# Optimization experiments

Measured on AMD Instinct MI355X. Metric: run time of the kernel, lower is better.

## Reference

```python
import jax, jax.numpy as jnp
import numpy as np
from jax import lax

# dims: B=2, C=dim=64, H=W=128 -> N=16384 tokens; d_inner=128, d_state=16, dt_rank=4, d_conv=4

def setup_inputs() -> dict:
    key = jax.random.key(0)
    ks = jax.random.split(key, 8)
    def n(k, shp, scale=0.02):
        return jax.random.normal(k, shp, jnp.float32) * scale
    d_inner, d_state, dt_rank = 128, 16, 4
    return {
        "x": jax.random.normal(ks[0], (2, 64, 128, 128), jnp.float32),
        "ln_w": jnp.ones((64,), jnp.float32),
        "ln_b": jnp.zeros((64,), jnp.float32),
        "in_proj_w": n(ks[1], (2 * d_inner, 64)),
        "conv_w": n(ks[2], (d_inner, 1, 4), 0.1),
        "conv_b": jnp.zeros((d_inner,), jnp.float32),
        "x_proj_w": n(ks[3], (dt_rank + 2 * d_state, d_inner)),
        "dt_proj_w": n(ks[4], (d_inner, dt_rank), 0.5),
        "dt_proj_b": n(ks[5], (d_inner,), 0.1),
        "A_log": jnp.log(jnp.broadcast_to(jnp.arange(1, d_state + 1, dtype=jnp.float32), (d_inner, d_state))),
        "D_param": jnp.ones((d_inner,), jnp.float32),
        "out_proj_w": n(ks[6], (64, d_inner)),
        "out_proj_b": jnp.zeros((64,), jnp.float32),
    }


def reference(x, ln_w, ln_b, in_proj_w, conv_w, conv_b, x_proj_w,
              dt_proj_w, dt_proj_b, A_log, D_param, out_proj_w, out_proj_b):
    B, C, H, W = x.shape
    d_inner = in_proj_w.shape[0] // 2
    d_state = A_log.shape[1]
    dt_rank = dt_proj_w.shape[1]
    eps = 1e-5

    # feature2token + channel LayerNorm (Restormer WithBias LN over C)
    t = x.reshape(B, C, H * W).transpose(0, 2, 1)  # [B, N, C]
    mu = jnp.mean(t, axis=-1, keepdims=True)
    var = jnp.var(t, axis=-1, keepdims=True)
    t = (t - mu) * lax.rsqrt(var + eps) * ln_w + ln_b

    # in_proj -> x, z
    xz = jnp.einsum('bnc,dc->bnd', t, in_proj_w)  # [B, N, 2*d_inner]
    x_in, z = jnp.split(xz, 2, axis=-1)

    # depthwise causal conv1d (k=4, pad left 3), then SiLU
    u = lax.conv_general_dilated(
        x_in.transpose(0, 2, 1), conv_w,
        window_strides=(1,), padding=[(3, 0)],
        feature_group_count=d_inner,
        dimension_numbers=('NCH', 'OIH', 'NCH'))
    u = jax.nn.silu(u + conv_b[None, :, None]).transpose(0, 2, 1)  # [B, N, d_inner]

    # x_proj -> dt, B, C of the SSM
    x_dbl = jnp.einsum('bnd,ed->bne', u, x_proj_w)
    dt_r = x_dbl[..., :dt_rank]
    Bmat = x_dbl[..., dt_rank:dt_rank + d_state]   # [B, N, d_state]
    Cmat = x_dbl[..., dt_rank + d_state:]          # [B, N, d_state]
    dt = jax.nn.softplus(jnp.einsum('bnr,dr->bnd', dt_r, dt_proj_w) + dt_proj_b)

    # selective scan: h_t = exp(dt*A) h_{t-1} + dt*B*u
    A = -jnp.exp(A_log)  # [d_inner, d_state]
    deltaA = jnp.exp(jnp.einsum('bnd,ds->bnds', dt, A))
    deltaBu = jnp.einsum('bnd,bns,bnd->bnds', dt, Bmat, u)

    def combine(c1, c2):
        a1, b1 = c1
        a2, b2 = c2
        return a2 * a1, a2 * b1 + b2

    _, h = lax.associative_scan(combine, (deltaA, deltaBu), axis=1)  # h: [B, N, d_inner, d_state]

    y = jnp.einsum('bnds,bns->bnd', h, Cmat) + u * D_param
    y = y * jax.nn.silu(z)
    out = jnp.einsum('bnd,cd->bnc', y, out_proj_w) + out_proj_b  # [B, N, C]

    # token2feature
    return out.transpose(0, 2, 1).reshape(B, C, H, W)
```

## Files before the change

kernel.cpp:

```cpp
#include <hip/hip_runtime.h>
#include <math.h>

#define NTOK 16384
#define DIN  128
#define NCH  512
#define CHL  32
#define NG   32
#define GCH  16

__device__ __forceinline__ float silu_f(float x)    { return x / (1.f + __expf(-x)); }
__device__ __forceinline__ float softplus_f(float x){ return (x > 20.f) ? x : log1pf(__expf(x)); }

__global__ __launch_bounds__(256) void k1_ln_inproj(
    const float* __restrict__ x, const float* __restrict__ lnw,
    const float* __restrict__ lnb, const float* __restrict__ Win,
    float* __restrict__ xin, float* __restrict__ zbuf)
{
  __shared__ __align__(16) float bufA[128*68];
  __shared__ __align__(16) float bufB[64*68];
  __shared__ float ps[256], pq[256], mu[64], rs[64];

  int t = threadIdx.x;
  int b  = blockIdx.x >> 8;
  int n0 = (blockIdx.x & 255) << 6;
  const float* xb = x + ((size_t)b*64)*NTOK;

  int tok = t & 63, quad = t >> 6;
  float s0 = 0.f, s1 = 0.f;
  for (int i = 0; i < 16; ++i) {
    int c = i*4 + quad;
    float v = xb[(size_t)c*NTOK + n0 + tok];
    bufA[c*68 + tok] = v;
    s0 += v; s1 += v*v;
  }
  ps[t] = s0; pq[t] = s1;
  __syncthreads();
  if (t < 64) {
    float m = ps[t] + ps[64+t] + ps[128+t] + ps[192+t];
    float q = pq[t] + pq[64+t] + pq[128+t] + pq[192+t];
    m *= 0.015625f;
    q = q*0.015625f - m*m;
    mu[t] = m; rs[t] = rsqrtf(q + 1e-5f);
  }
  __syncthreads();

  {
    int c = t & 63, tq = t >> 6;
    float wv = lnw[c], bv = lnb[c];
    const float4* A4 = (const float4*)bufA;
    #pragma unroll
    for (int i = 0; i < 4; ++i) {
      int tok4 = tq*4 + i;
      float4 f = A4[c*17 + tok4];
      float vals[4] = {f.x, f.y, f.z, f.w};
      #pragma unroll
      for (int k = 0; k < 4; ++k) {
        int tk = tok4*4 + k;
        bufB[tk*68 + c] = (vals[k] - mu[tk]) * rs[tk] * wv + bv;
      }
    }
  }

  int tokg = t & 15, dg = t >> 4;
  for (int half = 0; half < 2; ++half) {
    __syncthreads();
    for (int i = 0; i < 32; ++i) {
      int idx = i*256 + t;
      int c = idx & 63, dd = idx >> 6;
      bufA[dd*68 + c] = Win[((half<<7) + dd)*64 + c];
    }
    __syncthreads();
    float acc[4][8];
    #pragma unroll
    for (int i = 0; i < 4; ++i)
      #pragma unroll
      for (int j = 0; j < 8; ++j) acc[i][j] = 0.f;
    const float4* TB = (const float4*)bufB;
    const float4* WA = (const float4*)bufA;
    #pragma unroll 4
    for (int c4 = 0; c4 < 16; ++c4) {
      float4 tv[4], wv[8];
      #pragma unroll
      for (int i = 0; i < 4; ++i) tv[i] = TB[(tokg + 16*i)*17 + c4];
      #pragma unroll
      for (int j = 0; j < 8; ++j) wv[j] = WA[(dg + 16*j)*17 + c4];
      #pragma unroll
      for (int i = 0; i < 4; ++i)
        #pragma unroll
        for (int j = 0; j < 8; ++j)
          acc[i][j] += tv[i].x*wv[j].x + tv[i].y*wv[j].y
                     + tv[i].z*wv[j].z + tv[i].w*wv[j].w;
    }
    #pragma unroll
    for (int i = 0; i < 4; ++i) {
      long n = (long)b*NTOK + n0 + tokg + 16*i;
      #pragma unroll
      for (int j = 0; j < 8; ++j) {
        int d = dg + 16*j;
        if (half == 0) xin[n*128 + d] = acc[i][j];
        else           zbuf[n*128 + d] = silu_f(acc[i][j]);
      }
    }
  }
}

__global__ __launch_bounds__(256) void k2_conv(
    const float* __restrict__ xin, const float* __restrict__ cw,
    const float* __restrict__ cb, float* __restrict__ u)
{
  int t = threadIdx.x;
  int d = t & 127;
  long g0 = (long)blockIdx.x*16 + (t >> 7)*8;
  int n = (int)(g0 & (NTOK-1));
  float w0 = cw[d*4], w1 = cw[d*4+1], w2 = cw[d*4+2], w3 = cw[d*4+3];
  float cbv = cb[d];
  float xa = (n >= 3) ? xin[(g0-3)*128 + d] : 0.f;
  float xb = (n >= 2) ? xin[(g0-2)*128 + d] : 0.f;
  float xc = (n >= 1) ? xin[(g0-1)*128 + d] : 0.f;
  #pragma unroll
  for (int j = 0; j < 8; ++j) {
    float xd = xin[(g0+j)*128 + d];
    u[(g0+j)*128 + d] = silu_f(w0*xa + w1*xb + w2*xc + w3*xd + cbv);
    xa = xb; xb = xc; xc = xd;
  }
}

__global__ __launch_bounds__(256) void k3_xproj_dt(
    const float* __restrict__ u, const float* __restrict__ Wx,
    const float* __restrict__ Wdt, const float* __restrict__ db,
    float* __restrict__ dt, float* __restrict__ Bm, float* __restrict__ Cm)
{
  __shared__ __align__(16) float wx[36*128];
  __shared__ float wdtT[4*128];
  __shared__ __align__(16) float xdbl[64*40];
  int t = threadIdx.x;
  for (int i = t; i < 1152; i += 256)
    *(float4*)&wx[i*4] = *(const float4*)&Wx[i*4];
  for (int i = t; i < 512; i += 256)
    wdtT[(i&3)*128 + (i>>2)] = Wdt[i];
  __syncthreads();

  long tok0 = (long)blockIdx.x * 64;
  int tok = t & 63, grp = t >> 6;
  const float* urow = u + (tok0 + tok)*128;

  float acc[9];
  #pragma unroll
  for (int e = 0; e < 9; ++e) acc[e] = 0.f;
  #pragma unroll 8
  for (int d4 = 0; d4 < 32; ++d4) {
    float4 uv = *(const float4*)&urow[d4*4];
    #pragma unroll
    for (int e = 0; e < 9; ++e) {
      float4 wv = *(const float4*)&wx[(grp*9+e)*128 + d4*4];
      acc[e] += uv.x*wv.x + uv.y*wv.y + uv.z*wv.z + uv.w*wv.w;
    }
  }
  #pragma unroll
  for (int e = 0; e < 9; ++e) xdbl[tok*40 + grp*9 + e] = acc[e];
  __syncthreads();

  {
    int tk = t >> 2, q = t & 3;
    float4 bv = *(const float4*)&xdbl[tk*40 + 4  + q*4];
    float4 cv = *(const float4*)&xdbl[tk*40 + 20 + q*4];
    *(float4*)&Bm[(tok0+tk)*16 + q*4] = bv;
    *(float4*)&Cm[(tok0+tk)*16 + q*4] = cv;
  }
  int d = t & 127, th = t >> 7;
  float w0 = wdtT[d], w1 = wdtT[128+d], w2 = wdtT[256+d], w3 = wdtT[384+d];
  float bias = db[d];
  for (int j = 0; j < 32; ++j) {
    int tk = th*32 + j;
    float a = bias + xdbl[tk*40]*w0 + xdbl[tk*40+1]*w1
                   + xdbl[tk*40+2]*w2 + xdbl[tk*40+3]*w3;
    dt[(tok0+tk)*128 + d] = softplus_f(a);
  }
}

__global__ __launch_bounds__(128) void k4a_local(
    const float* __restrict__ dt, const float* __restrict__ u,
    const float* __restrict__ Bm, const float* __restrict__ Alog,
    float* __restrict__ carP, float* __restrict__ carH)
{
  int d = threadIdx.x;
  int b = blockIdx.x / NCH, ch = blockIdx.x % NCH;
  long nb = (long)b*NTOK + (long)ch*CHL;
  float A[16], h[16], P[16];
  #pragma unroll
  for (int k = 0; k < 4; ++k) {
    float4 a = *(const float4*)&Alog[d*16 + k*4];
    A[k*4+0] = -__expf(a.x); A[k*4+1] = -__expf(a.y);
    A[k*4+2] = -__expf(a.z); A[k*4+3] = -__expf(a.w);
  }
  #pragma unroll
  for (int s = 0; s < 16; ++s) { h[s] = 0.f; P[s] = 1.f; }
  for (int i = 0; i < CHL; ++i) {
    long n = nb + i;
    float dtv = dt[n*128 + d];
    float uv  = u [n*128 + d];
    float du  = dtv * uv;
    float Bv[16];
    #pragma unroll
    for (int k = 0; k < 4; ++k) {
      float4 v = *(const float4*)&Bm[n*16 + k*4];
      Bv[k*4]=v.x; Bv[k*4+1]=v.y; Bv[k*4+2]=v.z; Bv[k*4+3]=v.w;
    }
    #pragma unroll
    for (int s = 0; s < 16; ++s) {
      float dA = __expf(dtv * A[s]);
      h[s] = dA*h[s] + du*Bv[s];
      P[s] *= dA;
    }
  }
  long cbs = ((long)(b*NCH + ch)*128 + d) * 16;
  #pragma unroll
  for (int k = 0; k < 4; ++k) {
    *(float4*)&carP[cbs + k*4] = make_float4(P[k*4],P[k*4+1],P[k*4+2],P[k*4+3]);
    *(float4*)&carH[cbs + k*4] = make_float4(h[k*4],h[k*4+1],h[k*4+2],h[k*4+3]);
  }
}

__global__ __launch_bounds__(256) void k4b1_group(
    float* __restrict__ cP, float* __restrict__ cH,
    float* __restrict__ Pg, float* __restrict__ Hg)
{
  int idx = blockIdx.x*256 + threadIdx.x;
  int rem = idx & 2047;
  int g   = (idx >> 11) & (NG-1);
  int b   = idx >> 16;
  float P = 1.f, H = 0.f;
  long base = ((long)b*NCH + g*GCH)*2048 + rem;
  #pragma unroll 4
  for (int j = 0; j < GCH; ++j) {
    long a = base + (long)j*2048;
    float p = cP[a], h = cH[a];
    cP[a] = P; cH[a] = H;
    H = p*H + h;
    P = p*P;
  }
  long ga = ((long)b*NG + g)*2048 + rem;
  Pg[ga] = P; Hg[ga] = H;
}

__global__ __launch_bounds__(256) void k4b2_carry(
    const float* __restrict__ Pg, float* __restrict__ Hg)
{
  int idx = blockIdx.x*256 + threadIdx.x;
  int b = idx >> 11, rem = idx & 2047;
  float H = 0.f;
  #pragma unroll 4
  for (int g = 0; g < NG; ++g) {
    long a = ((long)b*NG + g)*2048 + rem;
    float p = Pg[a], h = Hg[a];
    Hg[a] = H;
    H = p*H + h;
  }
}

__global__ __launch_bounds__(128) void k4c_apply(
    const float* __restrict__ dt, const float* __restrict__ u,
    const float* __restrict__ Bm, const float* __restrict__ Cm,
    const float* __restrict__ Alog, const float* __restrict__ Dp,
    const float* __restrict__ zs, const float* __restrict__ pPre,
    const float* __restrict__ hPre, const float* __restrict__ Hg,
    float* __restrict__ yz)
{
  int d = threadIdx.x;
  int b = blockIdx.x / NCH, ch = blockIdx.x % NCH;
  long nb = (long)b*NTOK + (long)ch*CHL;
  float A[16], h[16];
  #pragma unroll
  for (int k = 0; k < 4; ++k) {
    float4 a = *(const float4*)&Alog[d*16 + k*4];
    A[k*4+0] = -__expf(a.x); A[k*4+1] = -__expf(a.y);
    A[k*4+2] = -__expf(a.z); A[k*4+3] = -__expf(a.w);
  }
  long cbs = ((long)(b*NCH + ch)*128 + d) * 16;
  long gbs = ((long)b*NG + (ch >> 4))*2048 + d*16;
  #pragma unroll
  for (int k = 0; k < 4; ++k) {
    float4 hp = *(const float4*)&hPre[cbs + k*4];
    float4 pp = *(const float4*)&pPre[cbs + k*4];
    float4 gi = *(const float4*)&Hg[gbs + k*4];
    h[k*4+0] = hp.x + pp.x*gi.x; h[k*4+1] = hp.y + pp.y*gi.y;
    h[k*4+2] = hp.z + pp.z*gi.z; h[k*4+3] = hp.w + pp.w*gi.w;
  }
  float Dv = Dp[d];
  for (int i = 0; i < CHL; ++i) {
    long n = nb + i;
    float dtv = dt[n*128 + d];
    float uv  = u [n*128 + d];
    float du  = dtv * uv;
    float Bv[16], Cv[16];
    #pragma unroll
    for (int k = 0; k < 4; ++k) {
      float4 v = *(const float4*)&Bm[n*16 + k*4];
      Bv[k*4]=v.x; Bv[k*4+1]=v.y; Bv[k*4+2]=v.z; Bv[k*4+3]=v.w;
      float4 w = *(const float4*)&Cm[n*16 + k*4];
      Cv[k*4]=w.x; Cv[k*4+1]=w.y; Cv[k*4+2]=w.z; Cv[k*4+3]=w.w;
    }
    float y = 0.f;
    #pragma unroll
    for (int s = 0; s < 16; ++s) {
      float dA = __expf(dtv * A[s]);
      h[s] = dA*h[s] + du*Bv[s];
      y += h[s]*Cv[s];
    }
    y = (y + uv*Dv) * zs[n*128 + d];
    yz[n*128 + d] = y;
  }
}

__global__ __launch_bounds__(256) void k6_outproj(
    const float* __restrict__ yz, const float* __restrict__ Wout,
    const float* __restrict__ ob, float* __restrict__ out)
{
  __shared__ __align__(16) float wo[64*132];
  __shared__ __align__(16) float yl[32*132];
  int t = threadIdx.x;
  long tok0 = (long)blockIdx.x * 32;
  for (int i = 0; i < 8; ++i) {
    int g = i*256 + t; int c = g >> 5, q = g & 31;
    *(float4*)&wo[c*132 + q*4] = *(const float4*)&Wout[c*128 + q*4];
  }
  for (int i = 0; i < 4; ++i) {
    int g = i*256 + t; int tok = g >> 5, q = g & 31;
    *(float4*)&yl[tok*132 + q*4] = *(const float4*)&yz[(tok0 + tok)*128 + q*4];
  }
  __syncthreads();
  int tp = t & 15;
  int tg = t >> 4;
  float acc[4][2] = {{0.f}};
  for (int d4 = 0; d4 < 32; ++d4) {
    float4 y0 = *(const float4*)&yl[tg*132 + d4*4];
    float4 y1 = *(const float4*)&yl[(tg+16)*132 + d4*4];
    #pragma unroll
    for (int cc = 0; cc < 4; ++cc) {
      float4 wv = *(const float4*)&wo[(tp + 16*cc)*132 + d4*4];
      acc[cc][0] += wv.x*y0.x + wv.y*y0.y + wv.z*y0.z + wv.w*y0.w;
      acc[cc][1] += wv.x*y1.x + wv.y*y1.y + wv.z*y1.z + wv.w*y1.w;
    }
  }
  int b  = (int)(tok0 / NTOK);
  long n0 = tok0 % NTOK;
  #pragma unroll
  for (int cc = 0; cc < 4; ++cc) {
    int c = tp + 16*cc;
    float bias = ob[c];
    out[((long)b*64 + c)*NTOK + n0 + tg     ] = acc[cc][0] + bias;
    out[((long)b*64 + c)*NTOK + n0 + tg + 16] = acc[cc][1] + bias;
  }
}

extern "C" void kernel_launch(void* const* d_in, const int* in_sizes, int n_in,
                              void* d_out, int out_size, void* d_ws, size_t ws_size,
                              hipStream_t stream)
{
  (void)in_sizes; (void)n_in; (void)out_size; (void)ws_size;
  const float* x    = (const float*)d_in[0];
  const float* lnw  = (const float*)d_in[1];
  const float* lnb  = (const float*)d_in[2];
  const float* Win  = (const float*)d_in[3];
  const float* cw   = (const float*)d_in[4];
  const float* cb   = (const float*)d_in[5];
  const float* Wx   = (const float*)d_in[6];
  const float* Wdt  = (const float*)d_in[7];
  const float* db   = (const float*)d_in[8];
  const float* Alog = (const float*)d_in[9];
  const float* Dp   = (const float*)d_in[10];
  const float* Wout = (const float*)d_in[11];
  const float* ob   = (const float*)d_in[12];
  float* out = (float*)d_out;

  float* w   = (float*)d_ws;
  float* xin = w;
  float* z   = w + 4194304;
  float* u   = w + 8388608;
  float* dt  = w + 12582912;
  float* Bm  = w + 16777216;
  float* Cm  = w + 17301504;
  float* cP  = w + 17825792;
  float* cH  = w + 19922944;
  float* Pg  = w + 22020096;
  float* Hg  = w + 22151168;

  k1_ln_inproj<<<512, 256, 0, stream>>>(x, lnw, lnb, Win, xin, z);
  k2_conv     <<<2048,256, 0, stream>>>(xin, cw, cb, u);
  k3_xproj_dt <<<512, 256, 0, stream>>>(u, Wx, Wdt, db, dt, Bm, Cm);
  k4a_local   <<<1024,128, 0, stream>>>(dt, u, Bm, Alog, cP, cH);
  k4b1_group  <<<512, 256, 0, stream>>>(cP, cH, Pg, Hg);
  k4b2_carry  <<<16,  256, 0, stream>>>(Pg, Hg);
  k4c_apply   <<<1024,128, 0, stream>>>(dt, u, Bm, Cm, Alog, Dp, z, cP, cH, Hg, xin);
  k6_outproj  <<<1024,256, 0, stream>>>(xin, Wout, ob, out);
}
```

Baseline: 158.0 us.

## Fuse causal conv into LN/in_proj kernel and out_proj into scan apply

The conv1d stage moves into the LayerNorm/in_proj kernel. Each block now recomputes LN and the x projection for three halo tokens and runs the depthwise conv from shared memory, so the xin intermediate is never written to or read from global memory. The out projection is fused into the scan-apply kernel, which stages y in shared memory and writes the output directly, removing the yz round trip and two launches. The cost is redundant halo computation and more shared memory per block, including 8K floats of Wout loaded per apply block, which may lower occupancy.

```diff
diff --git a/kernel.cpp b/kernel.cpp
--- a/kernel.cpp
+++ b/kernel.cpp
@@ -11,77 +11,94 @@
 __device__ __forceinline__ float silu_f(float x)    { return x / (1.f + __expf(-x)); }
 __device__ __forceinline__ float softplus_f(float x){ return (x > 20.f) ? x : log1pf(__expf(x)); }
 
-__global__ __launch_bounds__(256) void k1_ln_inproj(
+__global__ __launch_bounds__(256) void k12(
     const float* __restrict__ x, const float* __restrict__ lnw,
     const float* __restrict__ lnb, const float* __restrict__ Win,
-    float* __restrict__ xin, float* __restrict__ zbuf)
-{
-  __shared__ __align__(16) float bufA[128*68];
-  __shared__ __align__(16) float bufB[64*68];
-  __shared__ float ps[256], pq[256], mu[64], rs[64];
+    const float* __restrict__ cw, const float* __restrict__ cb,
+    float* __restrict__ zbuf, float* __restrict__ u)
+{
+  __shared__ __align__(16) float bufA[128*69];
+  __shared__ __align__(16) float bufB[67*68];
+  __shared__ float ps[256], pq[256];
+  __shared__ float mu[67], rs[67];
 
   int t = threadIdx.x;
   int b  = blockIdx.x >> 8;
   int n0 = (blockIdx.x & 255) << 6;
-  const float* xb = x + ((size_t)b*64)*NTOK;
+  const float* xb = x + (size_t)b*64*NTOK;
 
   int tok = t & 63, quad = t >> 6;
   float s0 = 0.f, s1 = 0.f;
   for (int i = 0; i < 16; ++i) {
     int c = i*4 + quad;
     float v = xb[(size_t)c*NTOK + n0 + tok];
-    bufA[c*68 + tok] = v;
+    bufA[c*68 + tok + 3] = v;
     s0 += v; s1 += v*v;
   }
   ps[t] = s0; pq[t] = s1;
-  __syncthreads();
+  float vh = 0.f;
+  if (t < 192) {
+    int c = t & 63, k = t >> 6;
+    int n = n0 - 3 + k;
+    vh = (n >= 0) ? xb[(size_t)c*NTOK + n] : 0.f;
+    bufA[c*68 + k] = vh;
+  }
+  __syncthreads();
+  if (t < 192) {
+    float a0 = vh, a1 = vh*vh;
+    #pragma unroll
+    for (int m = 1; m < 64; m <<= 1) { a0 += __shfl_xor(a0, m); a1 += __shfl_xor(a1, m); }
+    if ((t & 63) == 0) {
+      int k = t >> 6;
+      float m = a0 * 0.015625f;
+      float q = a1 * 0.015625f - m*m;
+      mu[k] = m; rs[k] = rsqrtf(q + 1e-5f);
+    }
+  }
   if (t < 64) {
     float m = ps[t] + ps[64+t] + ps[128+t] + ps[192+t];
     float q = pq[t] + pq[64+t] + pq[128+t] + pq[192+t];
     m *= 0.015625f;
     q = q*0.015625f - m*m;
-    mu[t] = m; rs[t] = rsqrtf(q + 1e-5f);
-  }
-  __syncthreads();
-
+    mu[t+3] = m; rs[t+3] = rsqrtf(q + 1e-5f);
+  }
+  __syncthreads();
   {
     int c = t & 63, tq = t >> 6;
     float wv = lnw[c], bv = lnb[c];
-    const float4* A4 = (const float4*)bufA;
-    #pragma unroll
-    for (int i = 0; i < 4; ++i) {
-      int tok4 = tq*4 + i;
-      float4 f = A4[c*17 + tok4];
-      float vals[4] = {f.x, f.y, f.z, f.w};
-      #pragma unroll
-      for (int k = 0; k < 4; ++k) {
-        int tk = tok4*4 + k;
-        bufB[tk*68 + c] = (vals[k] - mu[tk]) * rs[tk] * wv + bv;
+    #pragma unroll
+    for (int i = 0; i < 17; ++i) {
+      int tp = tq + 4*i;
+      if (tp < 67) {
+        float val = (tp < 3 && n0 == 0) ? 0.f
+                  : (bufA[c*68 + tp] - mu[tp]) * rs[tp] * wv + bv;
+        bufB[tp*68 + c] = val;
       }
     }
   }
 
   int tokg = t & 15, dg = t >> 4;
-  for (int half = 0; half < 2; ++half) {
-    __syncthreads();
-    for (int i = 0; i < 32; ++i) {
-      int idx = i*256 + t;
-      int c = idx & 63, dd = idx >> 6;
-      bufA[dd*68 + c] = Win[((half<<7) + dd)*64 + c];
-    }
-    __syncthreads();
+  const float4* TB = (const float4*)bufB;
+
+  __syncthreads();
+  for (int i = 0; i < 32; ++i) {
+    int idx = i*256 + t;
+    int c = idx & 63, dd = idx >> 6;
+    bufA[dd*68 + c] = Win[(128 + dd)*64 + c];
+  }
+  __syncthreads();
+  {
+    const float4* WA = (const float4*)bufA;
     float acc[4][8];
     #pragma unroll
     for (int i = 0; i < 4; ++i)
       #pragma unroll
       for (int j = 0; j < 8; ++j) acc[i][j] = 0.f;
-    const float4* TB = (const float4*)bufB;
-    const float4* WA = (const float4*)bufA;
     #pragma unroll 4
     for (int c4 = 0; c4 < 16; ++c4) {
       float4 tv[4], wv[8];
       #pragma unroll
-      for (int i = 0; i < 4; ++i) tv[i] = TB[(tokg + 16*i)*17 + c4];
+      for (int i = 0; i < 4; ++i) tv[i] = TB[(3 + tokg + 16*i)*17 + c4];
       #pragma unroll
       for (int j = 0; j < 8; ++j) wv[j] = WA[(dg + 16*j)*17 + c4];
       #pragma unroll
@@ -95,33 +112,73 @@
     for (int i = 0; i < 4; ++i) {
       long n = (long)b*NTOK + n0 + tokg + 16*i;
       #pragma unroll
-      for (int j = 0; j < 8; ++j) {
-        int d = dg + 16*j;
-        if (half == 0) xin[n*128 + d] = acc[i][j];
-        else           zbuf[n*128 + d] = silu_f(acc[i][j]);
+      for (int j = 0; j < 8; ++j)
+        zbuf[n*128 + dg + 16*j] = silu_f(acc[i][j]);
+    }
+  }
+
+  __syncthreads();
+  for (int i = 0; i < 32; ++i) {
+    int idx = i*256 + t;
+    int c = idx & 63, dd = idx >> 6;
+    bufA[dd*68 + c] = Win[dd*64 + c];
+  }
+  __syncthreads();
+  float acc[4][8], acch[8];
+  {
+    const float4* WA = (const float4*)bufA;
+    #pragma unroll
+    for (int i = 0; i < 4; ++i)
+      #pragma unroll
+      for (int j = 0; j < 8; ++j) acc[i][j] = 0.f;
+    #pragma unroll
+    for (int j = 0; j < 8; ++j) acch[j] = 0.f;
+    #pragma unroll 4
+    for (int c4 = 0; c4 < 16; ++c4) {
+      float4 tv[4], wv[8];
+      #pragma unroll
+      for (int i = 0; i < 4; ++i) tv[i] = TB[(3 + tokg + 16*i)*17 + c4];
+      #pragma unroll
+      for (int j = 0; j < 8; ++j) wv[j] = WA[(dg + 16*j)*17 + c4];
+      #pragma unroll
+      for (int i = 0; i < 4; ++i)
+        #pragma unroll
+        for (int j = 0; j < 8; ++j)
+          acc[i][j] += tv[i].x*wv[j].x + tv[i].y*wv[j].y
+                     + tv[i].z*wv[j].z + tv[i].w*wv[j].w;
+      if (tokg < 3) {
+        float4 th = TB[tokg*17 + c4];
+        #pragma unroll
+        for (int j = 0; j < 8; ++j)
+          acch[j] += th.x*wv[j].x + th.y*wv[j].y + th.z*wv[j].z + th.w*wv[j].w;
       }
     }
   }
-}
-
-__global__ __launch_bounds__(256) void k2_conv(
-    const float* __restrict__ xin, const float* __restrict__ cw,
-    const float* __restrict__ cb, float* __restrict__ u)
-{
-  int t = threadIdx.x;
-  int d = t & 127;
-  long g0 = (long)blockIdx.x*16 + (t >> 7)*8;
-  int n = (int)(g0 & (NTOK-1));
-  float w0 = cw[d*4], w1 = cw[d*4+1], w2 = cw[d*4+2], w3 = cw[d*4+3];
-  float cbv = cb[d];
-  float xa = (n >= 3) ? xin[(g0-3)*128 + d] : 0.f;
-  float xb = (n >= 2) ? xin[(g0-2)*128 + d] : 0.f;
-  float xc = (n >= 1) ? xin[(g0-1)*128 + d] : 0.f;
-  #pragma unroll
-  for (int j = 0; j < 8; ++j) {
-    float xd = xin[(g0+j)*128 + d];
-    u[(g0+j)*128 + d] = silu_f(w0*xa + w1*xb + w2*xc + w3*xd + cbv);
-    xa = xb; xb = xc; xc = xd;
+  __syncthreads();
+  #pragma unroll
+  for (int i = 0; i < 4; ++i)
+    #pragma unroll
+    for (int j = 0; j < 8; ++j)
+      bufA[(dg + 16*j)*69 + 3 + tokg + 16*i] = acc[i][j];
+  if (tokg < 3)
+    #pragma unroll
+    for (int j = 0; j < 8; ++j)
+      bufA[(dg + 16*j)*69 + tokg] = acch[j];
+  __syncthreads();
+
+  {
+    int d = t & 127, th = t >> 7;
+    float w0 = cw[d*4], w1 = cw[d*4+1], w2 = cw[d*4+2], w3 = cw[d*4+3];
+    float cbv = cb[d];
+    int base = d*69 + th*32;
+    float xa = bufA[base], xb2 = bufA[base+1], xc = bufA[base+2];
+    long g0 = (long)b*NTOK + n0 + th*32;
+    #pragma unroll
+    for (int j = 0; j < 32; ++j) {
+      float xd = bufA[base + j + 3];
+      u[(g0 + j)*128 + d] = silu_f(w0*xa + w1*xb2 + w2*xc + w3*xd + cbv);
+      xa = xb2; xb2 = xc; xc = xd;
+    }
   }
 }
 
@@ -258,15 +315,24 @@
   }
 }
 
-__global__ __launch_bounds__(128) void k4c_apply(
+__global__ __launch_bounds__(128) void k46(
     const float* __restrict__ dt, const float* __restrict__ u,
     const float* __restrict__ Bm, const float* __restrict__ Cm,
     const float* __restrict__ Alog, const float* __restrict__ Dp,
     const float* __restrict__ zs, const float* __restrict__ pPre,
     const float* __restrict__ hPre, const float* __restrict__ Hg,
-    float* __restrict__ yz)
-{
-  int d = threadIdx.x;
+    const float* __restrict__ Wout, const float* __restrict__ ob,
+    float* __restrict__ out)
+{
+  __shared__ __align__(16) float yl[32*132];
+  __shared__ __align__(16) float wo[64*128];
+  int t = threadIdx.x;
+  for (int i = 0; i < 16; ++i) {
+    int idx = i*128 + t;
+    *(float4*)&wo[idx*4] = *(const float4*)&Wout[idx*4];
+  }
+
+  int d = t;
   int b = blockIdx.x / NCH, ch = blockIdx.x % NCH;
   long nb = (long)b*NTOK + (long)ch*CHL;
   float A[16], h[16];
@@ -307,49 +373,30 @@
       h[s] = dA*h[s] + du*Bv[s];
       y += h[s]*Cv[s];
     }
-    y = (y + uv*Dv) * zs[n*128 + d];
-    yz[n*128 + d] = y;
-  }
-}
-
-__global__ __launch_bounds__(256) void k6_outproj(
-    const float* __restrict__ yz, const float* __restrict__ Wout,
-    const float* __restrict__ ob, float* __restrict__ out)
-{
-  __shared__ __align__(16) float wo[64*132];
-  __shared__ __align__(16) float yl[32*132];
-  int t = threadIdx.x;
-  long tok0 = (long)blockIdx.x * 32;
-  for (int i = 0; i < 8; ++i) {
-    int g = i*256 + t; int c = g >> 5, q = g & 31;
-    *(float4*)&wo[c*132 + q*4] = *(const float4*)&Wout[c*128 + q*4];
-  }
-  for (int i = 0; i < 4; ++i) {
-    int g = i*256 + t; int tok = g >> 5, q = g & 31;
-    *(float4*)&yl[tok*132 + q*4] = *(const float4*)&yz[(tok0 + tok)*128 + q*4];
-  }
-  __syncthreads();
-  int tp = t & 15;
-  int tg = t >> 4;
-  float acc[4][2] = {{0.f}};
-  for (int d4 = 0; d4 < 32; ++d4) {
-    float4 y0 = *(const float4*)&yl[tg*132 + d4*4];
-    float4 y1 = *(const float4*)&yl[(tg+16)*132 + d4*4];
-    #pragma unroll
-    for (int cc = 0; cc < 4; ++cc) {
-      float4 wv = *(const float4*)&wo[(tp + 16*cc)*132 + d4*4];
-      acc[cc][0] += wv.x*y0.x + wv.y*y0.y + wv.z*y0.z + wv.w*y0.w;
-      acc[cc][1] += wv.x*y1.x + wv.y*y1.y + wv.z*y1.z + wv.w*y1.w;
-    }
-  }
-  int b  = (int)(tok0 / NTOK);
-  long n0 = tok0 % NTOK;
-  #pragma unroll
-  for (int cc = 0; cc < 4; ++cc) {
-    int c = tp + 16*cc;
-    float bias = ob[c];
-    out[((long)b*64 + c)*NTOK + n0 + tg     ] = acc[cc][0] + bias;
-    out[((long)b*64 + c)*NTOK + n0 + tg + 16] = acc[cc][1] + bias;
+    yl[i*132 + d] = (y + uv*Dv) * zs[n*128 + d];
+  }
+  __syncthreads();
+
+  {
+    int tok = t & 31, cg = t >> 5;
+    float acc[16];
+    #pragma unroll
+    for (int cc = 0; cc < 16; ++cc) acc[cc] = 0.f;
+    #pragma unroll 4
+    for (int d4 = 0; d4 < 32; ++d4) {
+      float4 yv = *(const float4*)&yl[tok*132 + d4*4];
+      #pragma unroll
+      for (int cc = 0; cc < 16; ++cc) {
+        float4 wv = *(const float4*)&wo[(cg*16+cc)*128 + d4*4];
+        acc[cc] += yv.x*wv.x + yv.y*wv.y + yv.z*wv.z + yv.w*wv.w;
+      }
+    }
+    long col = (long)ch*CHL + tok;
+    #pragma unroll
+    for (int cc = 0; cc < 16; ++cc) {
+      int c = cg*16 + cc;
+      out[((long)b*64 + c)*NTOK + col] = acc[cc] + ob[c];
+    }
   }
 }
 
@@ -374,23 +421,21 @@
   float* out = (float*)d_out;
 
   float* w   = (float*)d_ws;
-  float* xin = w;
-  float* z   = w + 4194304;
-  float* u   = w + 8388608;
-  float* dt  = w + 12582912;
-  float* Bm  = w + 16777216;
-  float* Cm  = w + 17301504;
-  float* cP  = w + 17825792;
-  float* cH  = w + 19922944;
-  float* Pg  = w + 22020096;
-  float* Hg  = w + 22151168;
-
-  k1_ln_inproj<<<512, 256, 0, stream>>>(x, lnw, lnb, Win, xin, z);
-  k2_conv     <<<2048,256, 0, stream>>>(xin, cw, cb, u);
-  k3_xproj_dt <<<512, 256, 0, stream>>>(u, Wx, Wdt, db, dt, Bm, Cm);
-  k4a_local   <<<1024,128, 0, stream>>>(dt, u, Bm, Alog, cP, cH);
-  k4b1_group  <<<512, 256, 0, stream>>>(cP, cH, Pg, Hg);
-  k4b2_carry  <<<16,  256, 0, stream>>>(Pg, Hg);
-  k4c_apply   <<<1024,128, 0, stream>>>(dt, u, Bm, Cm, Alog, Dp, z, cP, cH, Hg, xin);
-  k6_outproj  <<<1024,256, 0, stream>>>(xin, Wout, ob, out);
-}
+  float* z   = w;
+  float* u   = w + 4194304;
+  float* dt  = w + 8388608;
+  float* Bm  = w + 12582912;
+  float* Cm  = w + 13107200;
+  float* cP  = w + 13631488;
+  float* cH  = w + 15728640;
+  float* Pg  = w + 17825792;
+  float* Hg  = w + 17956864;
+
+  k12        <<<512, 256, 0, stream>>>(x, lnw, lnb, Win, cw, cb, z, u);
+  k3_xproj_dt<<<512, 256, 0, stream>>>(u, Wx, Wdt, db, dt, Bm, Cm);
+  k4a_local  <<<1024,128, 0, stream>>>(dt, u, Bm, Alog, cP, cH);
+  k4b1_group <<<512, 256, 0, stream>>>(cP, cH, Pg, Hg);
+  k4b2_carry <<<16,  256, 0, stream>>>(Pg, Hg);
+  k46        <<<1024,128, 0, stream>>>(dt, u, Bm, Cm, Alog, Dp, z, cP, cH, Hg,
+                                       Wout, ob, out);
+}
```

Measured after the change: 182.7 us. 1.16x slower.

## Split scan state across thread pairs and quarter in_proj weight tiles

Applied to the files above, without the earlier changes.

The scan kernels now assign two threads per channel, each owning 8 of the 16 state elements, with the output reduced by a lane shuffle. This doubles the thread count and halves per-thread serial work and registers. k1 processes in_proj in four 64-row weight tiles instead of two 128-row ones, halving the shared-memory buffer and accumulator count to improve occupancy. The scan output goes to a separate yz buffer instead of overwriting xin, which adds workspace use, and each thread pair loads dt and u redundantly.

```diff
diff --git a/kernel.cpp b/kernel.cpp
--- a/kernel.cpp
+++ b/kernel.cpp
@@ -16,7 +16,7 @@
     const float* __restrict__ lnb, const float* __restrict__ Win,
     float* __restrict__ xin, float* __restrict__ zbuf)
 {
-  __shared__ __align__(16) float bufA[128*68];
+  __shared__ __align__(16) float bufA[64*68];
   __shared__ __align__(16) float bufB[64*68];
   __shared__ float ps[256], pq[256], mu[64], rs[64];
 
@@ -47,11 +47,10 @@
   {
     int c = t & 63, tq = t >> 6;
     float wv = lnw[c], bv = lnb[c];
-    const float4* A4 = (const float4*)bufA;
     #pragma unroll
     for (int i = 0; i < 4; ++i) {
       int tok4 = tq*4 + i;
-      float4 f = A4[c*17 + tok4];
+      float4 f = *(const float4*)&bufA[c*68 + tok4*4];
       float vals[4] = {f.x, f.y, f.z, f.w};
       #pragma unroll
       for (int k = 0; k < 4; ++k) {
@@ -62,32 +61,32 @@
   }
 
   int tokg = t & 15, dg = t >> 4;
-  for (int half = 0; half < 2; ++half) {
+  const float4* TB = (const float4*)bufB;
+  for (int q = 0; q < 4; ++q) {
     __syncthreads();
-    for (int i = 0; i < 32; ++i) {
+    for (int i = 0; i < 16; ++i) {
       int idx = i*256 + t;
       int c = idx & 63, dd = idx >> 6;
-      bufA[dd*68 + c] = Win[((half<<7) + dd)*64 + c];
+      bufA[dd*68 + c] = Win[(q*64 + dd)*64 + c];
     }
     __syncthreads();
-    float acc[4][8];
+    const float4* WA = (const float4*)bufA;
+    float acc[4][4];
     #pragma unroll
     for (int i = 0; i < 4; ++i)
       #pragma unroll
-      for (int j = 0; j < 8; ++j) acc[i][j] = 0.f;
-    const float4* TB = (const float4*)bufB;
-    const float4* WA = (const float4*)bufA;
+      for (int j = 0; j < 4; ++j) acc[i][j] = 0.f;
     #pragma unroll 4
     for (int c4 = 0; c4 < 16; ++c4) {
-      float4 tv[4], wv[8];
+      float4 tv[4], wv[4];
       #pragma unroll
       for (int i = 0; i < 4; ++i) tv[i] = TB[(tokg + 16*i)*17 + c4];
       #pragma unroll
-      for (int j = 0; j < 8; ++j) wv[j] = WA[(dg + 16*j)*17 + c4];
+      for (int j = 0; j < 4; ++j) wv[j] = WA[(dg + 16*j)*17 + c4];
       #pragma unroll
       for (int i = 0; i < 4; ++i)
         #pragma unroll
-        for (int j = 0; j < 8; ++j)
+        for (int j = 0; j < 4; ++j)
           acc[i][j] += tv[i].x*wv[j].x + tv[i].y*wv[j].y
                      + tv[i].z*wv[j].z + tv[i].w*wv[j].w;
     }
@@ -95,10 +94,10 @@
     for (int i = 0; i < 4; ++i) {
       long n = (long)b*NTOK + n0 + tokg + 16*i;
       #pragma unroll
-      for (int j = 0; j < 8; ++j) {
-        int d = dg + 16*j;
-        if (half == 0) xin[n*128 + d] = acc[i][j];
-        else           zbuf[n*128 + d] = silu_f(acc[i][j]);
+      for (int j = 0; j < 4; ++j) {
+        int dd = dg + 16*j;
+        if (q < 2) xin[n*128 + q*64 + dd] = acc[i][j];
+        else       zbuf[n*128 + (q-2)*64 + dd] = silu_f(acc[i][j]);
       }
     }
   }
@@ -178,44 +177,45 @@
   }
 }
 
-__global__ __launch_bounds__(128) void k4a_local(
+__global__ __launch_bounds__(256) void k4a_local(
     const float* __restrict__ dt, const float* __restrict__ u,
     const float* __restrict__ Bm, const float* __restrict__ Alog,
     float* __restrict__ carP, float* __restrict__ carH)
 {
-  int d = threadIdx.x;
+  int t = threadIdx.x;
+  int d = t >> 1, sh = t & 1;
   int b = blockIdx.x / NCH, ch = blockIdx.x % NCH;
   long nb = (long)b*NTOK + (long)ch*CHL;
-  float A[16], h[16], P[16];
-  #pragma unroll
-  for (int k = 0; k < 4; ++k) {
-    float4 a = *(const float4*)&Alog[d*16 + k*4];
+  float A[8], h[8], P[8];
+  #pragma unroll
+  for (int k = 0; k < 2; ++k) {
+    float4 a = *(const float4*)&Alog[d*16 + sh*8 + k*4];
     A[k*4+0] = -__expf(a.x); A[k*4+1] = -__expf(a.y);
     A[k*4+2] = -__expf(a.z); A[k*4+3] = -__expf(a.w);
   }
   #pragma unroll
-  for (int s = 0; s < 16; ++s) { h[s] = 0.f; P[s] = 1.f; }
+  for (int s = 0; s < 8; ++s) { h[s] = 0.f; P[s] = 1.f; }
   for (int i = 0; i < CHL; ++i) {
     long n = nb + i;
     float dtv = dt[n*128 + d];
     float uv  = u [n*128 + d];
     float du  = dtv * uv;
-    float Bv[16];
-    #pragma unroll
-    for (int k = 0; k < 4; ++k) {
-      float4 v = *(const float4*)&Bm[n*16 + k*4];
+    float Bv[8];
+    #pragma unroll
+    for (int k = 0; k < 2; ++k) {
+      float4 v = *(const float4*)&Bm[n*16 + sh*8 + k*4];
       Bv[k*4]=v.x; Bv[k*4+1]=v.y; Bv[k*4+2]=v.z; Bv[k*4+3]=v.w;
     }
     #pragma unroll
-    for (int s = 0; s < 16; ++s) {
+    for (int s = 0; s < 8; ++s) {
       float dA = __expf(dtv * A[s]);
       h[s] = dA*h[s] + du*Bv[s];
       P[s] *= dA;
     }
   }
-  long cbs = ((long)(b*NCH + ch)*128 + d) * 16;
-  #pragma unroll
-  for (int k = 0; k < 4; ++k) {
+  long cbs = ((long)(b*NCH + ch)*128 + d)*16 + sh*8;
+  #pragma unroll
+  for (int k = 0; k < 2; ++k) {
     *(float4*)&carP[cbs + k*4] = make_float4(P[k*4],P[k*4+1],P[k*4+2],P[k*4+3]);
     *(float4*)&carH[cbs + k*4] = make_float4(h[k*4],h[k*4+1],h[k*4+2],h[k*4+3]);
   }
@@ -258,7 +258,7 @@
   }
 }
 
-__global__ __launch_bounds__(128) void k4c_apply(
+__global__ __launch_bounds__(256) void k4c_apply(
     const float* __restrict__ dt, const float* __restrict__ u,
     const float* __restrict__ Bm, const float* __restrict__ Cm,
     const float* __restrict__ Alog, const float* __restrict__ Dp,
@@ -266,20 +266,21 @@
     const float* __restrict__ hPre, const float* __restrict__ Hg,
     float* __restrict__ yz)
 {
-  int d = threadIdx.x;
+  int t = threadIdx.x;
+  int d = t >> 1, sh = t & 1;
   int b = blockIdx.x / NCH, ch = blockIdx.x % NCH;
   long nb = (long)b*NTOK + (long)ch*CHL;
-  float A[16], h[16];
-  #pragma unroll
-  for (int k = 0; k < 4; ++k) {
-    float4 a = *(const float4*)&Alog[d*16 + k*4];
+  float A[8], h[8];
+  #pragma unroll
+  for (int k = 0; k < 2; ++k) {
+    float4 a = *(const float4*)&Alog[d*16 + sh*8 + k*4];
     A[k*4+0] = -__expf(a.x); A[k*4+1] = -__expf(a.y);
     A[k*4+2] = -__expf(a.z); A[k*4+3] = -__expf(a.w);
   }
-  long cbs = ((long)(b*NCH + ch)*128 + d) * 16;
-  long gbs = ((long)b*NG + (ch >> 4))*2048 + d*16;
-  #pragma unroll
-  for (int k = 0; k < 4; ++k) {
+  long cbs = ((long)(b*NCH + ch)*128 + d)*16 + sh*8;
+  long gbs = ((long)b*NG + (ch >> 4))*2048 + d*16 + sh*8;
+  #pragma unroll
+  for (int k = 0; k < 2; ++k) {
     float4 hp = *(const float4*)&hPre[cbs + k*4];
     float4 pp = *(const float4*)&pPre[cbs + k*4];
     float4 gi = *(const float4*)&Hg[gbs + k*4];
@@ -292,23 +293,24 @@
     float dtv = dt[n*128 + d];
     float uv  = u [n*128 + d];
     float du  = dtv * uv;
-    float Bv[16], Cv[16];
-    #pragma unroll
-    for (int k = 0; k < 4; ++k) {
-      float4 v = *(const float4*)&Bm[n*16 + k*4];
+    float Bv[8], Cv[8];
+    #pragma unroll
+    for (int k = 0; k < 2; ++k) {
+      float4 v = *(const float4*)&Bm[n*16 + sh*8 + k*4];
       Bv[k*4]=v.x; Bv[k*4+1]=v.y; Bv[k*4+2]=v.z; Bv[k*4+3]=v.w;
-      float4 w = *(const float4*)&Cm[n*16 + k*4];
+      float4 w = *(const float4*)&Cm[n*16 + sh*8 + k*4];
       Cv[k*4]=w.x; Cv[k*4+1]=w.y; Cv[k*4+2]=w.z; Cv[k*4+3]=w.w;
     }
     float y = 0.f;
     #pragma unroll
-    for (int s = 0; s < 16; ++s) {
+    for (int s = 0; s < 8; ++s) {
       float dA = __expf(dtv * A[s]);
       h[s] = dA*h[s] + du*Bv[s];
       y += h[s]*Cv[s];
     }
-    y = (y + uv*Dv) * zs[n*128 + d];
-    yz[n*128 + d] = y;
+    y += __shfl_xor(y, 1);
+    if (sh == 0)
+      yz[n*128 + d] = (y + uv*Dv) * zs[n*128 + d];
   }
 }
 
@@ -384,13 +386,14 @@
   float* cH  = w + 19922944;
   float* Pg  = w + 22020096;
   float* Hg  = w + 22151168;
+  float* yz  = w + 22282240;
 
   k1_ln_inproj<<<512, 256, 0, stream>>>(x, lnw, lnb, Win, xin, z);
   k2_conv     <<<2048,256, 0, stream>>>(xin, cw, cb, u);
   k3_xproj_dt <<<512, 256, 0, stream>>>(u, Wx, Wdt, db, dt, Bm, Cm);
-  k4a_local   <<<1024,128, 0, stream>>>(dt, u, Bm, Alog, cP, cH);
+  k4a_local   <<<1024,256, 0, stream>>>(dt, u, Bm, Alog, cP, cH);
   k4b1_group  <<<512, 256, 0, stream>>>(cP, cH, Pg, Hg);
   k4b2_carry  <<<16,  256, 0, stream>>>(Pg, Hg);
-  k4c_apply   <<<1024,128, 0, stream>>>(dt, u, Bm, Cm, Alog, Dp, z, cP, cH, Hg, xin);
-  k6_outproj  <<<1024,256, 0, stream>>>(xin, Wout, ob, out);
-}
+  k4c_apply   <<<1024,256, 0, stream>>>(dt, u, Bm, Cm, Alog, Dp, z, cP, cH, Hg, yz);
+  k6_outproj  <<<1024,256, 0, stream>>>(yz, Wout, ob, out);
+}
```

New measurement: 155.7 us. Within noise of the previous version (-1.4%).
